# Kernel optimization log

Measured on AMD Instinct MI355X. Metric: run time of the kernel, lower is better.

## Reference

```python
import jax, jax.numpy as jnp
import numpy as np

B = 8192          # batch rows
C_IN = 4096       # total input channels
G = 8             # number of clusters
CG = C_IN // G    # channels per cluster (arrangement.shape[0])
J = 512           # j_rank per cluster (output width per cluster)


def setup_inputs() -> dict:
    key = jax.random.key(0)
    kx, kp, kw, kb = jax.random.split(key, 4)
    x = jax.random.normal(kx, (B, C_IN), dtype=jnp.float32)
    # arrangements: a random permutation of all input channels split into G groups,
    # mimicking channel-clustering assignments (each channel used exactly once)
    perm = jax.random.permutation(kp, C_IN)
    arrangements = perm.reshape(G, CG).astype(jnp.int64)
    # per-group nn.Linear weights: torch layout (out_features, in_features)
    weights = jax.random.normal(kw, (G, J, CG), dtype=jnp.float32) * (1.0 / np.sqrt(CG))
    bias = jax.random.normal(kb, (G, J), dtype=jnp.float32) * 0.02
    return {"x": x, "arrangements": arrangements, "weights": weights, "bias": bias}


def reference(x, arrangements, weights, bias):
    # Gather each cluster's channels: x[:, arrangements] -> [B, G, CG]
    xg = jnp.take(x, arrangements, axis=1)
    # Per-group linear (torch Linear: y = x @ W.T + b), batched over groups,
    # then concat along feature dim -> [B, G*J]
    out = jnp.einsum('bgc,gjc->bgj', xg, weights) + bias[None, :, :]
    return out.reshape(x.shape[0], -1)
```

## Files before the change

### kernel.cpp

```cpp
#include <hip/hip_runtime.h>
#include <hip/hip_bf16.h>

#define B_ROWS 8192
#define C_IN   4096
#define G_GRP  8
#define CG     512
#define J_RANK 512

#define BM 256
#define BN 256
#define BK 64
#define NKT (CG / BK)

#define RPB    8
#define PERM_BLOCKS (B_ROWS / RPB)

typedef __attribute__((ext_vector_type(8))) short bf16x8;
typedef __attribute__((ext_vector_type(4))) float f32x4;
typedef __attribute__((ext_vector_type(8))) unsigned short u16x8;

struct ushort4v { unsigned short x, y, z, w; };

__device__ __forceinline__ unsigned short f2bf(float f) {
    unsigned int u = __float_as_uint(f);
    unsigned int r = (u + 0x7FFFu + ((u >> 16) & 1u)) >> 16;
    return (unsigned short)r;
}

__global__ __launch_bounds__(256) void convert_w_kernel(
    const float* __restrict__ w, unsigned short* __restrict__ wb, int n4) {
    int i = blockIdx.x * 256 + threadIdx.x;
    if (i >= n4) return;
    float4 v = ((const float4*)w)[i];
    ushort4v o;
    o.x = f2bf(v.x); o.y = f2bf(v.y); o.z = f2bf(v.z); o.w = f2bf(v.w);
    ((ushort4v*)wb)[i] = o;
}

__global__ __launch_bounds__(256) void permute_x_kernel(
    const float* __restrict__ x, const int* __restrict__ arr,
    unsigned short* __restrict__ xp) {
    __shared__ float buf[3][C_IN];
    const int tid  = threadIdx.x;
    const int row0 = blockIdx.x * RPB;

    const bool is64 = (arr[1] == 0 && arr[3] == 0 && arr[5] == 0 && arr[7] == 0);

    int sidx[16];
#pragma unroll
    for (int pass = 0; pass < 2; ++pass)
#pragma unroll
        for (int k = 0; k < 8; ++k) {
            int p = pass * 2048 + tid * 8 + k;
            sidx[pass * 8 + k] = is64 ? arr[2 * p] : arr[p];
        }

#define PSTAGE(bufi, r)                                                      \
    do {                                                                     \
        const float* src_ = x + (size_t)(row0 + (r)) * C_IN;                 \
        _Pragma("unroll")                                                    \
        for (int i_ = 0; i_ < 4; ++i_) {                                     \
            int c_ = i_ * 256 + tid;                                         \
            __builtin_amdgcn_global_load_lds(                                \
                (const __attribute__((address_space(1))) unsigned int*)      \
                    (src_ + c_ * 4),                                         \
                (__attribute__((address_space(3))) unsigned int*)            \
                    (&buf[bufi][0] + c_ * 4),                                \
                16, 0, 0);                                                   \
        }                                                                    \
    } while (0)

    PSTAGE(0, 0);
    PSTAGE(1, 1);
    PSTAGE(2, 2);

#pragma unroll
    for (int r = 0; r < RPB; ++r) {
        if (r == 0)            asm volatile("s_waitcnt vmcnt(8)"  ::: "memory");
        else if (r == 1)       asm volatile("s_waitcnt vmcnt(10)" ::: "memory");
        else if (r == RPB - 2) asm volatile("s_waitcnt vmcnt(8)"  ::: "memory");
        else if (r == RPB - 1) asm volatile("s_waitcnt vmcnt(4)"  ::: "memory");
        else                   asm volatile("s_waitcnt vmcnt(12)" ::: "memory");
        __builtin_amdgcn_s_barrier();
        __builtin_amdgcn_sched_barrier(0);

        const int bi = r % 3;
        unsigned short* orow = xp + (size_t)(row0 + r) * C_IN;
#pragma unroll
        for (int pass = 0; pass < 2; ++pass) {
            u16x8 o;
#pragma unroll
            for (int k = 0; k < 8; ++k)
                o[k] = f2bf(buf[bi][sidx[pass * 8 + k]]);
            *(u16x8*)(orow + pass * 2048 + tid * 8) = o;
        }

        __builtin_amdgcn_sched_barrier(0);
        __builtin_amdgcn_s_barrier();
        if (r + 3 < RPB) PSTAGE(bi, r + 3);
    }
#undef PSTAGE
}

__global__ __launch_bounds__(512, 2) void gemm_kernel(
    const unsigned short* __restrict__ Xp,
    const unsigned short* __restrict__ Wb,
    const float* __restrict__ bias,
    float* __restrict__ out) {
    __shared__ unsigned short ldsA[3][BM * BK];
    __shared__ unsigned short ldsB[2][BN * BK];

    const int tid = threadIdx.x;
    const int g   = blockIdx.x & 7;
    const int idx = blockIdx.x >> 3;
    const int mt  = idx >> 1;
    const int nt  = idx & 1;

    const int l   = tid & 63;
    const int wv  = tid >> 6;
    const int wr  = wv >> 2;
    const int wc  = wv & 3;
    const int lr  = l & 15;
    const int lkq = l >> 4;
    const int rx  = lr & 7;

    const unsigned short* Ab = Xp + (size_t)(mt * BM) * C_IN + g * CG;
    const unsigned short* Bb = Wb + (size_t)g * J_RANK * CG + (size_t)(nt * BN) * CG;

    f32x4 acc[8][4];
#pragma unroll
    for (int m = 0; m < 8; ++m)
#pragma unroll
        for (int n = 0; n < 4; ++n) acc[m][n] = (f32x4){0.f, 0.f, 0.f, 0.f};

    const int aRow = (wr * 128 + lr) * BK;
    const int bRow = (wc * 64 + lr) * BK;
    int coff[2];
#pragma unroll
    for (int kk = 0; kk < 2; ++kk) coff[kk] = (((kk << 2) | lkq) ^ rx) * 8;

#define STAGE_A(h, kt_)                                                       \
    do { const int p_ = (kt_) % 3;                                            \
        _Pragma("unroll")                                                     \
        for (int i_ = 0; i_ < 2; ++i_) {                                      \
            int c_ = i_ * 512 + tid;                                          \
            int rl_ = c_ >> 3, gc_ = (c_ & 7) ^ (rl_ & 7);                    \
            __builtin_amdgcn_global_load_lds(                                 \
                (const __attribute__((address_space(1))) unsigned int*)       \
                    (Ab + (size_t)((h) * 128 + rl_) * C_IN + (kt_) * BK + gc_ * 8), \
                (__attribute__((address_space(3))) unsigned int*)             \
                    (&ldsA[p_][0] + (h) * 8192 + c_ * 8),                     \
                16, 0, 0);                                                    \
        }                                                                     \
    } while (0)

#define STAGE_B(h, kt_)                                                       \
    do { const int p_ = (kt_) & 1;                                            \
        _Pragma("unroll")                                                     \
        for (int i_ = 0; i_ < 2; ++i_) {                                      \
            int c_ = i_ * 512 + tid;                                          \
            int rl_ = c_ >> 3, gc_ = (c_ & 7) ^ (rl_ & 7);                    \
            __builtin_amdgcn_global_load_lds(                                 \
                (const __attribute__((address_space(1))) unsigned int*)       \
                    (Bb + (size_t)((h) * 128 + rl_) * CG + (kt_) * BK + gc_ * 8), \
                (__attribute__((address_space(3))) unsigned int*)             \
                    (&ldsB[p_][0] + (h) * 8192 + c_ * 8),                     \
                16, 0, 0);                                                    \
        }                                                                     \
    } while (0)

#define LDA(m_, kk_) (*(const bf16x8*)&ldsA[bufA][aRow + (m_) * 16 * BK + coff[kk_]])
#define LDB(n_, kk_) (*(const bf16x8*)&ldsB[bufB][bRow + (n_) * 16 * BK + coff[kk_]])

#define MFMA_Q(q_)                                                            \
    _Pragma("unroll")                                                         \
    for (int mm_ = 0; mm_ < 2; ++mm_)                                         \
    _Pragma("unroll")                                                         \
    for (int n_ = 0; n_ < 4; ++n_)                                            \
    _Pragma("unroll")                                                         \
    for (int kk_ = 0; kk_ < 2; ++kk_)                                         \
        acc[2 * (q_) + mm_][n_] = __builtin_amdgcn_mfma_f32_16x16x32_bf16(    \
            af[mm_][kk_], bfr[n_][kk_], acc[2 * (q_) + mm_][n_], 0, 0, 0);

#define PHASE_TAIL()                                                          \
    __builtin_amdgcn_s_barrier();                                             \
    asm volatile("s_waitcnt lgkmcnt(0)" ::: "memory");                        \
    __builtin_amdgcn_sched_barrier(0);                                        \
    __builtin_amdgcn_s_setprio(1)

#define PHASE_END()                                                           \
    __builtin_amdgcn_s_setprio(0);                                            \
    __builtin_amdgcn_s_barrier()

    STAGE_A(0, 0); STAGE_A(1, 0); STAGE_B(0, 0); STAGE_B(1, 0);
    STAGE_A(0, 1); STAGE_A(1, 1); STAGE_B(0, 1); STAGE_B(1, 1);
    asm volatile("s_waitcnt vmcnt(8)" ::: "memory");
    __builtin_amdgcn_s_barrier();

    bf16x8 bfr[4][2], af[2][2];

    for (int kt = 0; kt < NKT; ++kt) {
        const int bufA = kt % 3;
        const int bufB = kt & 1;

#pragma unroll
        for (int n = 0; n < 4; ++n)
#pragma unroll
            for (int kk = 0; kk < 2; ++kk) bfr[n][kk] = LDB(n, kk);
#pragma unroll
        for (int mm = 0; mm < 2; ++mm)
#pragma unroll
            for (int kk = 0; kk < 2; ++kk) af[mm][kk] = LDA(mm, kk);
        if (kt + 2 < NKT) STAGE_A(0, kt + 2);
        PHASE_TAIL();
        MFMA_Q(0);
        PHASE_END();

#pragma unroll
        for (int mm = 0; mm < 2; ++mm)
#pragma unroll
            for (int kk = 0; kk < 2; ++kk) af[mm][kk] = LDA(2 + mm, kk);
        if (kt + 2 < NKT) STAGE_A(1, kt + 2);
        PHASE_TAIL();
        MFMA_Q(1);
        PHASE_END();

#pragma unroll
        for (int mm = 0; mm < 2; ++mm)
#pragma unroll
            for (int kk = 0; kk < 2; ++kk) af[mm][kk] = LDA(4 + mm, kk);
        if (kt + 2 < NKT) STAGE_B(0, kt + 2);
        PHASE_TAIL();
        MFMA_Q(2);
        PHASE_END();

#pragma unroll
        for (int mm = 0; mm < 2; ++mm)
#pragma unroll
            for (int kk = 0; kk < 2; ++kk) af[mm][kk] = LDA(6 + mm, kk);
        if (kt + 2 < NKT) STAGE_B(1, kt + 2);
        if (kt <= NKT - 3)      asm volatile("s_waitcnt vmcnt(8)" ::: "memory");
        else if (kt == NKT - 2) asm volatile("s_waitcnt vmcnt(0)" ::: "memory");
        PHASE_TAIL();
        MFMA_Q(3);
        PHASE_END();
    }
#undef STAGE_A
#undef STAGE_B
#undef LDA
#undef LDB
#undef MFMA_Q
#undef PHASE_TAIL
#undef PHASE_END

    const int r0 = mt * BM + wr * 128 + (lkq << 2);
    const int cbase = nt * BN + wc * 64 + lr;
#pragma unroll
    for (int n = 0; n < 4; ++n) {
        int col = cbase + n * 16;
        float bv = bias[g * J_RANK + col];
#pragma unroll
        for (int m = 0; m < 8; ++m) {
            int row = r0 + m * 16;
            float* op = out + (size_t)row * C_IN + g * J_RANK + col;
#pragma unroll
            for (int r = 0; r < 4; ++r)
                __builtin_nontemporal_store(acc[m][n][r] + bv, op + (size_t)r * C_IN);
        }
    }
}

extern "C" void kernel_launch(void* const* d_in, const int* in_sizes, int n_in,
                              void* d_out, int out_size, void* d_ws, size_t ws_size,
                              hipStream_t stream) {
    const float* x    = (const float*)d_in[0];
    const int*   arr  = (const int*)d_in[1];
    const float* w    = (const float*)d_in[2];
    const float* bias = (const float*)d_in[3];
    float* out = (float*)d_out;

    unsigned short* xp = (unsigned short*)d_ws;
    unsigned short* wb = xp + (size_t)B_ROWS * C_IN;

    hipLaunchKernelGGL(convert_w_kernel, dim3((G_GRP * J_RANK * CG / 4 + 255) / 256),
                       dim3(256), 0, stream, w, wb, G_GRP * J_RANK * CG / 4);
    hipLaunchKernelGGL(permute_x_kernel, dim3(PERM_BLOCKS), dim3(256), 0, stream,
                       x, arr, xp);
    hipLaunchKernelGGL(gemm_kernel,
                       dim3(G_GRP * (B_ROWS / BM) * (J_RANK / BN)), dim3(512),
                       0, stream, xp, wb, bias, out);
}
```

Before: 113.3 us.

## Shrink GEMM block tile to 128x256 with BK 32 for higher occupancy

Halves the M tile and the K step of the grouped bf16 GEMM and raises the launch-bounds occupancy hint from 2 to 4 blocks per CU. The staging swizzle, the LDS fragment addressing and the per-k-step phases are rewritten for 32-wide K slices, with two MFMA phases per step instead of four. The epilogue switches from nontemporal stores to plain stores. The aim is more resident blocks and a smaller register footprint to hide latency. In exchange, each block reuses operand tiles less, takes twice as many k-iterations with more barriers, and its LDS use may still prevent four blocks from fitting per CU.

```diff
diff --git a/kernel.cpp b/kernel.cpp
--- a/kernel.cpp
+++ b/kernel.cpp
@@ -7,9 +7,9 @@
 #define CG     512
 #define J_RANK 512
 
-#define BM 256
+#define BM 128
 #define BN 256
-#define BK 64
+#define BK 32
 #define NKT (CG / BK)
 
 #define RPB    8
@@ -102,7 +102,7 @@
 #undef PSTAGE
 }
 
-__global__ __launch_bounds__(512, 2) void gemm_kernel(
+__global__ __launch_bounds__(512, 4) void gemm_kernel(
     const unsigned short* __restrict__ Xp,
     const unsigned short* __restrict__ Wb,
     const float* __restrict__ bias,
@@ -122,65 +122,47 @@
     const int wc  = wv & 3;
     const int lr  = l & 15;
     const int lkq = l >> 4;
-    const int rx  = lr & 7;
 
     const unsigned short* Ab = Xp + (size_t)(mt * BM) * C_IN + g * CG;
     const unsigned short* Bb = Wb + (size_t)g * J_RANK * CG + (size_t)(nt * BN) * CG;
 
-    f32x4 acc[8][4];
-#pragma unroll
-    for (int m = 0; m < 8; ++m)
+    f32x4 acc[4][4];
+#pragma unroll
+    for (int m = 0; m < 4; ++m)
 #pragma unroll
         for (int n = 0; n < 4; ++n) acc[m][n] = (f32x4){0.f, 0.f, 0.f, 0.f};
 
-    const int aRow = (wr * 128 + lr) * BK;
-    const int bRow = (wc * 64 + lr) * BK;
-    int coff[2];
-#pragma unroll
-    for (int kk = 0; kk < 2; ++kk) coff[kk] = (((kk << 2) | lkq) ^ rx) * 8;
-
-#define STAGE_A(h, kt_)                                                       \
+    const int coff = (lkq ^ ((lr >> 2) & 3)) * 8;
+
+#define STAGE_A(kt_)                                                          \
     do { const int p_ = (kt_) % 3;                                            \
-        _Pragma("unroll")                                                     \
-        for (int i_ = 0; i_ < 2; ++i_) {                                      \
-            int c_ = i_ * 512 + tid;                                          \
-            int rl_ = c_ >> 3, gc_ = (c_ & 7) ^ (rl_ & 7);                    \
-            __builtin_amdgcn_global_load_lds(                                 \
-                (const __attribute__((address_space(1))) unsigned int*)       \
-                    (Ab + (size_t)((h) * 128 + rl_) * C_IN + (kt_) * BK + gc_ * 8), \
-                (__attribute__((address_space(3))) unsigned int*)             \
-                    (&ldsA[p_][0] + (h) * 8192 + c_ * 8),                     \
-                16, 0, 0);                                                    \
-        }                                                                     \
+        int c_ = tid;                                                         \
+        int rl_ = c_ >> 2, gc_ = (c_ & 3) ^ ((rl_ >> 2) & 3);                 \
+        __builtin_amdgcn_global_load_lds(                                     \
+            (const __attribute__((address_space(1))) unsigned int*)           \
+                (Ab + (size_t)rl_ * C_IN + (kt_) * BK + gc_ * 8),             \
+            (__attribute__((address_space(3))) unsigned int*)                 \
+                (&ldsA[p_][0] + c_ * 8),                                      \
+            16, 0, 0);                                                        \
     } while (0)
 
-#define STAGE_B(h, kt_)                                                       \
+#define STAGE_B(kt_)                                                          \
     do { const int p_ = (kt_) & 1;                                            \
         _Pragma("unroll")                                                     \
         for (int i_ = 0; i_ < 2; ++i_) {                                      \
             int c_ = i_ * 512 + tid;                                          \
-            int rl_ = c_ >> 3, gc_ = (c_ & 7) ^ (rl_ & 7);                    \
+            int rl_ = c_ >> 2, gc_ = (c_ & 3) ^ ((rl_ >> 2) & 3);             \
             __builtin_amdgcn_global_load_lds(                                 \
                 (const __attribute__((address_space(1))) unsigned int*)       \
-                    (Bb + (size_t)((h) * 128 + rl_) * CG + (kt_) * BK + gc_ * 8), \
+                    (Bb + (size_t)rl_ * CG + (kt_) * BK + gc_ * 8),           \
                 (__attribute__((address_space(3))) unsigned int*)             \
-                    (&ldsB[p_][0] + (h) * 8192 + c_ * 8),                     \
+                    (&ldsB[p_][0] + c_ * 8),                                  \
                 16, 0, 0);                                                    \
         }                                                                     \
     } while (0)
 
-#define LDA(m_, kk_) (*(const bf16x8*)&ldsA[bufA][aRow + (m_) * 16 * BK + coff[kk_]])
-#define LDB(n_, kk_) (*(const bf16x8*)&ldsB[bufB][bRow + (n_) * 16 * BK + coff[kk_]])
-
-#define MFMA_Q(q_)                                                            \
-    _Pragma("unroll")                                                         \
-    for (int mm_ = 0; mm_ < 2; ++mm_)                                         \
-    _Pragma("unroll")                                                         \
-    for (int n_ = 0; n_ < 4; ++n_)                                            \
-    _Pragma("unroll")                                                         \
-    for (int kk_ = 0; kk_ < 2; ++kk_)                                         \
-        acc[2 * (q_) + mm_][n_] = __builtin_amdgcn_mfma_f32_16x16x32_bf16(    \
-            af[mm_][kk_], bfr[n_][kk_], acc[2 * (q_) + mm_][n_], 0, 0, 0);
+#define LDA(m_) (*(const bf16x8*)&ldsA[bufA][(wr * 64 + (m_) * 16 + lr) * BK + coff])
+#define LDB(n_) (*(const bf16x8*)&ldsB[bufB][(wc * 64 + (n_) * 16 + lr) * BK + coff])
 
 #define PHASE_TAIL()                                                          \
     __builtin_amdgcn_s_barrier();                                             \
@@ -192,80 +174,63 @@
     __builtin_amdgcn_s_setprio(0);                                            \
     __builtin_amdgcn_s_barrier()
 
-    STAGE_A(0, 0); STAGE_A(1, 0); STAGE_B(0, 0); STAGE_B(1, 0);
-    STAGE_A(0, 1); STAGE_A(1, 1); STAGE_B(0, 1); STAGE_B(1, 1);
-    asm volatile("s_waitcnt vmcnt(8)" ::: "memory");
+    STAGE_A(0); STAGE_B(0);
+    STAGE_A(1); STAGE_B(1);
+    asm volatile("s_waitcnt vmcnt(3)" ::: "memory");
     __builtin_amdgcn_s_barrier();
 
-    bf16x8 bfr[4][2], af[2][2];
+    bf16x8 bfr[4], af[2];
 
     for (int kt = 0; kt < NKT; ++kt) {
         const int bufA = kt % 3;
         const int bufB = kt & 1;
 
 #pragma unroll
-        for (int n = 0; n < 4; ++n)
-#pragma unroll
-            for (int kk = 0; kk < 2; ++kk) bfr[n][kk] = LDB(n, kk);
+        for (int n = 0; n < 4; ++n) bfr[n] = LDB(n);
+        af[0] = LDA(0); af[1] = LDA(1);
+        if (kt + 2 < NKT) STAGE_A(kt + 2);
+        PHASE_TAIL();
 #pragma unroll
         for (int mm = 0; mm < 2; ++mm)
 #pragma unroll
-            for (int kk = 0; kk < 2; ++kk) af[mm][kk] = LDA(mm, kk);
-        if (kt + 2 < NKT) STAGE_A(0, kt + 2);
-        PHASE_TAIL();
-        MFMA_Q(0);
+            for (int n = 0; n < 4; ++n)
+                acc[mm][n] = __builtin_amdgcn_mfma_f32_16x16x32_bf16(
+                    af[mm], bfr[n], acc[mm][n], 0, 0, 0);
         PHASE_END();
 
-#pragma unroll
-        for (int mm = 0; mm < 2; ++mm)
-#pragma unroll
-            for (int kk = 0; kk < 2; ++kk) af[mm][kk] = LDA(2 + mm, kk);
-        if (kt + 2 < NKT) STAGE_A(1, kt + 2);
-        PHASE_TAIL();
-        MFMA_Q(1);
-        PHASE_END();
-
-#pragma unroll
-        for (int mm = 0; mm < 2; ++mm)
-#pragma unroll
-            for (int kk = 0; kk < 2; ++kk) af[mm][kk] = LDA(4 + mm, kk);
-        if (kt + 2 < NKT) STAGE_B(0, kt + 2);
-        PHASE_TAIL();
-        MFMA_Q(2);
-        PHASE_END();
-
-#pragma unroll
-        for (int mm = 0; mm < 2; ++mm)
-#pragma unroll
-            for (int kk = 0; kk < 2; ++kk) af[mm][kk] = LDA(6 + mm, kk);
-        if (kt + 2 < NKT) STAGE_B(1, kt + 2);
-        if (kt <= NKT - 3)      asm volatile("s_waitcnt vmcnt(8)" ::: "memory");
+        af[0] = LDA(2); af[1] = LDA(3);
+        if (kt + 2 < NKT) STAGE_B(kt + 2);
+        if (kt <= NKT - 3)      asm volatile("s_waitcnt vmcnt(3)" ::: "memory");
         else if (kt == NKT - 2) asm volatile("s_waitcnt vmcnt(0)" ::: "memory");
         PHASE_TAIL();
-        MFMA_Q(3);
+#pragma unroll
+        for (int mm = 0; mm < 2; ++mm)
+#pragma unroll
+            for (int n = 0; n < 4; ++n)
+                acc[2 + mm][n] = __builtin_amdgcn_mfma_f32_16x16x32_bf16(
+                    af[mm], bfr[n], acc[2 + mm][n], 0, 0, 0);
         PHASE_END();
     }
 #undef STAGE_A
 #undef STAGE_B
 #undef LDA
 #undef LDB
-#undef MFMA_Q
 #undef PHASE_TAIL
 #undef PHASE_END
 
-    const int r0 = mt * BM + wr * 128 + (lkq << 2);
+    const int r0 = mt * BM + wr * 64 + (lkq << 2);
     const int cbase = nt * BN + wc * 64 + lr;
 #pragma unroll
     for (int n = 0; n < 4; ++n) {
         int col = cbase + n * 16;
         float bv = bias[g * J_RANK + col];
 #pragma unroll
-        for (int m = 0; m < 8; ++m) {
+        for (int m = 0; m < 4; ++m) {
             int row = r0 + m * 16;
             float* op = out + (size_t)row * C_IN + g * J_RANK + col;
 #pragma unroll
             for (int r = 0; r < 4; ++r)
-                __builtin_nontemporal_store(acc[m][n][r] + bv, op + (size_t)r * C_IN);
+                op[(size_t)r * C_IN] = acc[m][n][r] + bv;
         }
     }
 }
```

Measured after the change: 105.9 us. 1.07x faster.
